# Optimization experiments

Measured on AMD Instinct MI355X. Metric: run time of the kernel, lower is better.

## Reference

```python
import jax, jax.numpy as jnp
import numpy as np

H = 4        # no_heads
C = 32       # c_hidden per head
CQ = 128     # c_q = c_k = c_v
N = 256      # pair dim / seq len
B = 1


def setup_inputs() -> dict:
    key = jax.random.key(0)
    ks = jax.random.split(key, 8)
    q_x = jax.random.normal(ks[0], (B, N, N, CQ), dtype=jnp.float32)
    kv_x = jax.random.normal(ks[1], (B, N, N, CQ), dtype=jnp.float32)
    mask_bias = jnp.zeros((B, N, 1, 1, N), dtype=jnp.float32)
    pair_bias = jax.random.normal(ks[2], (B, 1, H, N, N), dtype=jnp.float32)
    s = 1.0 / np.sqrt(CQ)
    w_q = jax.random.normal(ks[3], (H * C, CQ), dtype=jnp.float32) * s
    w_k = jax.random.normal(ks[4], (H * C, CQ), dtype=jnp.float32) * s
    w_v = jax.random.normal(ks[5], (H * C, CQ), dtype=jnp.float32) * s
    w_g = jax.random.normal(ks[6], (H * C, CQ), dtype=jnp.float32) * s
    w_o = jax.random.normal(ks[7], (CQ, H * C), dtype=jnp.float32) * s
    return {"q_x": q_x, "kv_x": kv_x, "mask_bias": mask_bias,
            "pair_bias": pair_bias, "w_q": w_q, "w_k": w_k, "w_v": w_v,
            "w_g": w_g, "w_o": w_o}


def reference(q_x, kv_x, mask_bias, pair_bias, w_q, w_k, w_v, w_g, w_o):
    # project: [B, N, Q, c] -> [B, N, H, Q, C]
    def proj(x, w):
        y = jnp.einsum('...qc,dc->...qd', x, w)            # [B,N,Q,H*C]
        y = y.reshape(*y.shape[:-1], H, C)                 # [B,N,Q,H,C]
        return jnp.swapaxes(y, -2, -3)                     # [B,N,H,Q,C]

    q = proj(q_x, w_q) / jnp.sqrt(jnp.asarray(C, q_x.dtype))
    k = proj(kv_x, w_k)
    v = proj(kv_x, w_v)

    # scores [B, N, H, Q, K] with both biases added pre-softmax
    a = jnp.einsum('...hqd,...hkd->...hqk', q, k) + mask_bias + pair_bias
    a = jax.nn.softmax(a, axis=-1)
    o = jnp.einsum('...hqk,...hkd->...hqd', a, v)          # [B,N,H,Q,C]
    o = jnp.swapaxes(o, -2, -3)                            # [B,N,Q,H,C]
    o = o.reshape(*o.shape[:-2], H * C)                    # [B,N,Q,H*C]

    g = jax.nn.sigmoid(jnp.einsum('...qc,dc->...qd', q_x, w_g))
    o = o * g
    return jnp.einsum('...qd,cd->...qc', o, w_o)           # [B,N,Q,c_q]
```

## Files before the change

kernel.cpp:

```cpp
#include <hip/hip_runtime.h>
#include <hip/hip_bf16.h>

#define H 4
#define C 32
#define CQ 128
#define NSEQ 256
#define HC 128

typedef __bf16 bf16;
typedef __bf16 bf16x8 __attribute__((ext_vector_type(8)));
typedef __bf16 bf16x4 __attribute__((ext_vector_type(4)));
typedef float f32x4 __attribute__((ext_vector_type(4)));

#define MFMA16(a, b, c) __builtin_amdgcn_mfma_f32_16x16x32_bf16(a, b, c, 0, 0, 0)

#define LOG2E 1.4426950408889634f

__device__ __forceinline__ bf16x8 cvt8(float4 a, float4 b) {
    return (bf16x8){(bf16)a.x, (bf16)a.y, (bf16)a.z, (bf16)a.w,
                    (bf16)b.x, (bf16)b.y, (bf16)b.z, (bf16)b.w};
}

__global__ __launch_bounds__(256) void prep_weights(const float* __restrict__ wq,
                                                    const float* __restrict__ wk,
                                                    const float* __restrict__ wv,
                                                    const float* __restrict__ wg,
                                                    const float* __restrict__ wo,
                                                    bf16* __restrict__ dst) {
    const int m = blockIdx.y;
    const float* src = (m == 0) ? wq : (m == 1) ? wk : (m == 2) ? wv : (m == 3) ? wg : wo;
    int i = blockIdx.x * 256 + threadIdx.x;
    float4 v = ((const float4*)src)[i];
    bf16x4 b = {(bf16)v.x, (bf16)v.y, (bf16)v.z, (bf16)v.w};
    ((bf16x4*)(dst + (size_t)m * 16384))[i] = b;
}

__global__ __launch_bounds__(512) void proj_all(const float* __restrict__ qx,
                                                const float* __restrict__ kvx,
                                                const bf16* __restrict__ wbf,
                                                bf16* __restrict__ qo,
                                                bf16* __restrict__ go,
                                                bf16* __restrict__ ko,
                                                bf16* __restrict__ vo) {
    __shared__ bf16 w1s[128][136];
    __shared__ bf16 w2s[128][136];
    __shared__ bf16 xs[2][64][136];

    const int t = threadIdx.x;
    const int mode = blockIdx.y;

    const float* x = mode ? kvx : qx;
    const bf16* w1 = wbf + (mode ? 1 : 0) * 16384;
    const bf16* w2 = wbf + (mode ? 2 : 3) * 16384;
    bf16* o1 = mode ? ko : qo;
    bf16* o2 = mode ? vo : go;

    const int row_blk = blockIdx.x * 256;
    const int sr = t >> 3, sc = (t & 7) * 16;

    #pragma unroll
    for (int i = t; i < 2048; i += 512) {
        int row = i >> 4, col = (i & 15) * 8;
        *(bf16x8*)&w1s[row][col] = *(const bf16x8*)&w1[row * CQ + col];
        *(bf16x8*)&w2s[row][col] = *(const bf16x8*)&w2[row * CQ + col];
    }
    {
        const float* p = x + (size_t)(row_blk + sr) * CQ + sc;
        float4 v0 = *(const float4*)p, v1 = *(const float4*)(p + 4);
        float4 v2 = *(const float4*)(p + 8), v3 = *(const float4*)(p + 12);
        *(bf16x8*)&xs[0][sr][sc] = cvt8(v0, v1);
        *(bf16x8*)&xs[0][sr][sc + 8] = cvt8(v2, v3);
    }
    __syncthreads();

    const int w = t >> 6, l = t & 63, lr = l & 15, lg = l >> 4;

    bf16x8 a1[4], a2[4];
    #pragma unroll
    for (int ks = 0; ks < 4; ks++) {
        a1[ks] = *(const bf16x8*)&w1s[w * 16 + lr][ks * 32 + lg * 8];
        a2[ks] = *(const bf16x8*)&w2s[w * 16 + lr][ks * 32 + lg * 8];
    }

    const float qscale = 0.17677669529663687f * LOG2E;

    #pragma unroll 1
    for (int it = 0; it < 4; it++) {
        const int cur = it & 1;

        float4 n0, n1, n2, n3;
        if (it < 3) {
            const float* p = x + (size_t)(row_blk + (it + 1) * 64 + sr) * CQ + sc;
            n0 = *(const float4*)p;
            n1 = *(const float4*)(p + 4);
            n2 = *(const float4*)(p + 8);
            n3 = *(const float4*)(p + 12);
        }

        #pragma unroll
        for (int rt = 0; rt < 4; rt++) {
            bf16x8 b[4];
            #pragma unroll
            for (int ks = 0; ks < 4; ks++)
                b[ks] = *(const bf16x8*)&xs[cur][rt * 16 + lr][ks * 32 + lg * 8];

            f32x4 acc1 = (f32x4)0.f, acc2 = (f32x4)0.f;
            #pragma unroll
            for (int ks = 0; ks < 4; ks++) {
                acc1 = MFMA16(a1[ks], b[ks], acc1);
                acc2 = MFMA16(a2[ks], b[ks], acc2);
            }

            bf16x4 st1, st2;
            #pragma unroll
            for (int r = 0; r < 4; r++) {
                float v1 = acc1[r], v2 = acc2[r];
                if (mode == 0) {
                    v1 *= qscale;
                    v2 = __builtin_amdgcn_rcpf(1.f + __builtin_amdgcn_exp2f(-v2 * LOG2E));
                }
                st1[r] = (bf16)v1;
                st2[r] = (bf16)v2;
            }
            const size_t obase =
                (size_t)(row_blk + it * 64 + rt * 16 + lr) * HC + w * 16 + lg * 4;
            *(bf16x4*)&o1[obase] = st1;
            *(bf16x4*)&o2[obase] = st2;
        }

        if (it < 3) {
            *(bf16x8*)&xs[cur ^ 1][sr][sc] = cvt8(n0, n1);
            *(bf16x8*)&xs[cur ^ 1][sr][sc + 8] = cvt8(n2, n3);
        }
        __syncthreads();
    }
}

__global__ __launch_bounds__(512) void attn_kernel(const bf16* __restrict__ qw,
                                                   const bf16* __restrict__ kw,
                                                   const bf16* __restrict__ vw,
                                                   const bf16* __restrict__ gw,
                                                   const float* __restrict__ pair_bias,
                                                   const float* __restrict__ mask_bias,
                                                   bf16* __restrict__ ow) {
    const int wg = blockIdx.x;
    const int swz = ((wg & 7) << 8) + (wg >> 3);
    const int qc2 = swz & 1;
    const int n1 = (swz >> 1) & 255;
    const int h = swz >> 9;

    __shared__ bf16 klds[256][40];
    __shared__ bf16 vts[32][256];
    __shared__ bf16 ps[8][16][76];

    const int t = threadIdx.x;

    {
        const size_t base = ((size_t)n1 * NSEQ) * HC + (size_t)h * C;
        const int rr = t >> 2, cc4 = t & 3, ch = cc4 * 8;
        #pragma unroll
        for (int p = 0; p < 2; p++) {
            int row = p * 128 + rr;
            bf16x8 kv = *(const bf16x8*)&kw[base + (size_t)row * HC + ch];
            *(bf16x8*)&klds[row][ch] = kv;
            bf16x8 vv = *(const bf16x8*)&vw[base + (size_t)row * HC + ch];
            #pragma unroll
            for (int j = 0; j < 8; j++) {
                int colw = row ^ (cc4 << 4) ^ (j << 3);
                vts[ch + j][colw] = vv[j];
            }
        }
    }

    const int w = t >> 6, l = t & 63, lr = l & 15, lg = l >> 4;
    const int qbase = qc2 * 128 + w * 16;

    bf16x8 qf = *(const bf16x8*)&qw[((size_t)(n1 * NSEQ + qbase + lr)) * HC + h * C + lg * 8];

    const float* pb = pair_bias + (size_t)h * NSEQ * NSEQ;
    const float* mb = mask_bias + (size_t)n1 * NSEQ;

    f32x4 s[16];
    #pragma unroll
    for (int kt = 0; kt < 16; kt++) {
        float mbk = mb[kt * 16 + lr] * LOG2E;
        #pragma unroll
        for (int r = 0; r < 4; r++)
            s[kt][r] = fmaf(pb[(size_t)(qbase + lg * 4 + r) * NSEQ + kt * 16 + lr],
                            LOG2E, mbk);
    }

    __syncthreads();

    #pragma unroll
    for (int kt = 0; kt < 16; kt++) {
        bf16x8 kf = *(const bf16x8*)&klds[kt * 16 + lr][lg * 8];
        s[kt] = MFMA16(qf, kf, s[kt]);
    }

    float pinv[4];
    #pragma unroll
    for (int r = 0; r < 4; r++) {
        float sum = 0.f;
        #pragma unroll
        for (int kt = 0; kt < 16; kt++) {
            float e = __builtin_amdgcn_exp2f(s[kt][r]);
            s[kt][r] = e;
            sum += e;
        }
        #pragma unroll
        for (int msk = 8; msk >= 1; msk >>= 1) sum += __shfl_xor(sum, msk, 64);
        pinv[r] = __builtin_amdgcn_rcpf(sum);
    }

    f32x4 o[2];
    o[0] = (f32x4)0.f;
    o[1] = (f32x4)0.f;
    #pragma unroll
    for (int qtr = 0; qtr < 4; qtr++) {
        #pragma unroll
        for (int kt2 = 0; kt2 < 4; kt2++) {
            #pragma unroll
            for (int r = 0; r < 4; r++)
                ps[w][lg * 4 + r][kt2 * 16 + lr] = (bf16)s[qtr * 4 + kt2][r];
        }
        #pragma unroll
        for (int kh = 0; kh < 2; kh++) {
            bf16x8 pf = *(const bf16x8*)&ps[w][lr][kh * 32 + lg * 8];
            #pragma unroll
            for (int ct = 0; ct < 2; ct++) {
                int g2 = (2 * ct + (lr >> 3)) & 3;
                int col0 = (qtr * 64 + kh * 32 + lg * 8) ^ (g2 << 4) ^ ((lr & 7) << 3);
                bf16x8 vf = *(const bf16x8*)&vts[ct * 16 + lr][col0];
                o[ct] = MFMA16(pf, vf, o[ct]);
            }
        }
    }

    #pragma unroll
    for (int ct = 0; ct < 2; ct++) {
        #pragma unroll
        for (int r = 0; r < 4; r++) {
            size_t idx = ((size_t)(n1 * NSEQ + qbase + lg * 4 + r)) * HC + (size_t)h * C +
                         ct * 16 + lr;
            float gv = (float)gw[idx];
            ow[idx] = (bf16)(o[ct][r] * pinv[r] * gv);
        }
    }
}

__global__ __launch_bounds__(512) void out_proj(const bf16* __restrict__ og,
                                                const bf16* __restrict__ wo,
                                                float* __restrict__ out) {
    __shared__ bf16 ws[128][136];
    __shared__ bf16 xs[2][64][136];

    const int t = threadIdx.x;
    const int row_blk = blockIdx.x * 256;
    const int sr = t >> 3, sc = (t & 7) * 16;

    #pragma unroll
    for (int i = t; i < 2048; i += 512) {
        int row = i >> 4, col = (i & 15) * 8;
        *(bf16x8*)&ws[row][col] = *(const bf16x8*)&wo[row * CQ + col];
    }
    {
        const bf16* p = og + (size_t)(row_blk + sr) * HC + sc;
        *(bf16x8*)&xs[0][sr][sc] = *(const bf16x8*)p;
        *(bf16x8*)&xs[0][sr][sc + 8] = *(const bf16x8*)(p + 8);
    }
    __syncthreads();

    const int w = t >> 6, l = t & 63, lr = l & 15, lg = l >> 4;

    bf16x8 a[4];
    #pragma unroll
    for (int ks = 0; ks < 4; ks++)
        a[ks] = *(const bf16x8*)&ws[w * 16 + lr][ks * 32 + lg * 8];

    #pragma unroll 1
    for (int it = 0; it < 4; it++) {
        const int cur = it & 1;

        bf16x8 m0, m1;
        if (it < 3) {
            const bf16* p = og + (size_t)(row_blk + (it + 1) * 64 + sr) * HC + sc;
            m0 = *(const bf16x8*)p;
            m1 = *(const bf16x8*)(p + 8);
        }

        #pragma unroll
        for (int rt = 0; rt < 4; rt++) {
            bf16x8 b[4];
            #pragma unroll
            for (int ks = 0; ks < 4; ks++)
                b[ks] = *(const bf16x8*)&xs[cur][rt * 16 + lr][ks * 32 + lg * 8];

            f32x4 acc = (f32x4)0.f;
            #pragma unroll
            for (int ks = 0; ks < 4; ks++)
                acc = MFMA16(a[ks], b[ks], acc);

            *(float4*)&out[(size_t)(row_blk + it * 64 + rt * 16 + lr) * CQ + w * 16 + lg * 4] =
                (float4){acc[0], acc[1], acc[2], acc[3]};
        }

        if (it < 3) {
            *(bf16x8*)&xs[cur ^ 1][sr][sc] = m0;
            *(bf16x8*)&xs[cur ^ 1][sr][sc + 8] = m1;
        }
        __syncthreads();
    }
}

extern "C" void kernel_launch(void* const* d_in, const int* in_sizes, int n_in,
                              void* d_out, int out_size, void* d_ws, size_t ws_size,
                              hipStream_t stream) {
    const float* q_x = (const float*)d_in[0];
    const float* kv_x = (const float*)d_in[1];
    const float* mask_bias = (const float*)d_in[2];
    const float* pair_bias = (const float*)d_in[3];
    const float* w_q = (const float*)d_in[4];
    const float* w_k = (const float*)d_in[5];
    const float* w_v = (const float*)d_in[6];
    const float* w_g = (const float*)d_in[7];
    const float* w_o = (const float*)d_in[8];

    const size_t M = (size_t)NSEQ * NSEQ;
    bf16* wbf = (bf16*)d_ws;
    bf16* qws = wbf + 5 * 16384;
    bf16* gws = qws + M * HC;
    bf16* kws = gws + M * HC;
    bf16* vws = kws + M * HC;
    bf16* ows = vws + M * HC;

    prep_weights<<<dim3(16, 5), 256, 0, stream>>>(w_q, w_k, w_v, w_g, w_o, wbf);
    proj_all<<<dim3(256, 2), 512, 0, stream>>>(q_x, kv_x, wbf, qws, gws, kws, vws);
    attn_kernel<<<dim3(2048), 512, 0, stream>>>(qws, kws, vws, gws, pair_bias,
                                                mask_bias, ows);
    out_proj<<<dim3(256), 512, 0, stream>>>(ows, wbf + 4 * 16384, (float*)d_out);
}
```

Before: 83.27 us.

## Transpose QK^T MFMA so each lane holds a query row, vectorizing bias loads and softmax

```diff
diff --git a/kernel.cpp b/kernel.cpp
--- a/kernel.cpp
+++ b/kernel.cpp
@@ -177,17 +177,19 @@
 
     bf16x8 qf = *(const bf16x8*)&qw[((size_t)(n1 * NSEQ + qbase + lr)) * HC + h * C + lg * 8];
 
-    const float* pb = pair_bias + (size_t)h * NSEQ * NSEQ;
+    const float* pbrow = pair_bias + (size_t)h * NSEQ * NSEQ + (size_t)(qbase + lr) * NSEQ;
     const float* mb = mask_bias + (size_t)n1 * NSEQ;
 
     f32x4 s[16];
     #pragma unroll
     for (int kt = 0; kt < 16; kt++) {
-        float mbk = mb[kt * 16 + lr] * LOG2E;
+        float4 pv = *(const float4*)&pbrow[kt * 16 + lg * 4];
+        float4 mv = *(const float4*)&mb[kt * 16 + lg * 4];
+        const float* pvp = (const float*)&pv;
+        const float* mvp = (const float*)&mv;
         #pragma unroll
         for (int r = 0; r < 4; r++)
-            s[kt][r] = fmaf(pb[(size_t)(qbase + lg * 4 + r) * NSEQ + kt * 16 + lr],
-                            LOG2E, mbk);
+            s[kt][r] = (pvp[r] + mvp[r]) * LOG2E;
     }
 
     __syncthreads();
@@ -195,23 +197,24 @@
     #pragma unroll
     for (int kt = 0; kt < 16; kt++) {
         bf16x8 kf = *(const bf16x8*)&klds[kt * 16 + lr][lg * 8];
-        s[kt] = MFMA16(qf, kf, s[kt]);
-    }
-
-    float pinv[4];
-    #pragma unroll
-    for (int r = 0; r < 4; r++) {
-        float sum = 0.f;
-        #pragma unroll
-        for (int kt = 0; kt < 16; kt++) {
-            float e = __builtin_amdgcn_exp2f(s[kt][r]);
-            s[kt][r] = e;
-            sum += e;
-        }
-        #pragma unroll
-        for (int msk = 8; msk >= 1; msk >>= 1) sum += __shfl_xor(sum, msk, 64);
-        pinv[r] = __builtin_amdgcn_rcpf(sum);
-    }
+        s[kt] = MFMA16(kf, qf, s[kt]);
+    }
+
+    #pragma unroll
+    for (int kt = 0; kt < 16; kt++)
+        #pragma unroll
+        for (int r = 0; r < 4; r++)
+            s[kt][r] = __builtin_amdgcn_exp2f(s[kt][r]);
+
+    f32x4 t0 = (s[0] + s[1]) + (s[2] + s[3]);
+    f32x4 t1 = (s[4] + s[5]) + (s[6] + s[7]);
+    f32x4 t2 = (s[8] + s[9]) + (s[10] + s[11]);
+    f32x4 t3 = (s[12] + s[13]) + (s[14] + s[15]);
+    f32x4 tv = (t0 + t1) + (t2 + t3);
+    float sum = (tv[0] + tv[1]) + (tv[2] + tv[3]);
+    sum += __shfl_xor(sum, 16, 64);
+    sum += __shfl_xor(sum, 32, 64);
+    const float pinv = __builtin_amdgcn_rcpf(sum);
 
     f32x4 o[2];
     o[0] = (f32x4)0.f;
@@ -220,9 +223,12 @@
     for (int qtr = 0; qtr < 4; qtr++) {
         #pragma unroll
         for (int kt2 = 0; kt2 < 4; kt2++) {
+            const int kt = qtr * 4 + kt2;
+            bf16x4 pk;
             #pragma unroll
             for (int r = 0; r < 4; r++)
-                ps[w][lg * 4 + r][kt2 * 16 + lr] = (bf16)s[qtr * 4 + kt2][r];
+                pk[r] = (bf16)s[kt][r];
+            *(bf16x4*)&ps[w][lr][kt2 * 16 + lg * 4] = pk;
         }
         #pragma unroll
         for (int kh = 0; kh < 2; kh++) {
@@ -237,6 +243,10 @@
         }
     }
 
+    float pr[4];
+    #pragma unroll
+    for (int r = 0; r < 4; r++) pr[r] = __shfl(pinv, lg * 4 + r, 64);
+
     #pragma unroll
     for (int ct = 0; ct < 2; ct++) {
         #pragma unroll
@@ -244,7 +254,7 @@
             size_t idx = ((size_t)(n1 * NSEQ + qbase + lg * 4 + r)) * HC + (size_t)h * C +
                          ct * 16 + lr;
             float gv = (float)gw[idx];
-            ow[idx] = (bf16)(o[ct][r] * pinv[r] * gv);
+            ow[idx] = (bf16)(o[ct][r] * pr[r] * gv);
         }
     }
 }
```

Result: slower. 103.9 us (+24.7%).
